# Optimization experiments

Measured on AMD Instinct MI355X. Metric: run time of the kernel, lower is better.

## Reference

```python
import jax, jax.numpy as jnp
import numpy as np

B, N, C = 256, 25, 256          # batch, joints, in_features
H = 256                          # hidden_features (MLP hidden = H // 2 = 128)


def _build_chain_paths(n):
    """Flatten shortest paths of a chain skeleton (parent[i]=i-1) into
    (heads, ends, pair_ids): edge k of path i->j contributes
    src[:, ends[e]] - src[:, heads[e]] accumulated into pair i*n+j."""
    heads, ends, pair = [], [], []
    for i in range(n):
        for j in range(n):
            step = 1 if j >= i else -1
            cur = i
            while cur != j:
                heads.append(cur)
                ends.append(cur + step)
                pair.append(i * n + j)
                cur += step
    return (np.asarray(heads, np.int32), np.asarray(ends, np.int32),
            np.asarray(pair, np.int32))


def setup_inputs() -> dict:
    key = jax.random.key(0)
    k_src, k_w1, k_w2 = jax.random.split(key, 3)
    heads, ends, pair_ids = _build_chain_paths(N)  # E = 5200 for N=25
    src = jax.random.normal(k_src, (B, N, C), dtype=jnp.float32)
    # torch Linear weights: [out, in], no bias for both edgefeat linears
    W1 = jax.random.normal(k_w1, (H // 2, C), dtype=jnp.float32) / np.sqrt(C)
    W2 = jax.random.normal(k_w2, (1, H // 2), dtype=jnp.float32) / np.sqrt(H // 2)
    alpha = jnp.full((1,), 0.25, dtype=jnp.float32)  # PReLU init
    return {"src": src, "heads": jnp.asarray(heads), "ends": jnp.asarray(ends),
            "pair_ids": jnp.asarray(pair_ids), "W1": W1, "alpha": alpha, "W2": W2}


def reference(src, heads, ends, pair_ids, W1, alpha, W2):
    b, n, c = src.shape
    # gather-subtract along every path edge: [B, E, C]
    diff = src[:, ends, :] - src[:, heads, :]
    # accumulate per (i, j) pair: segment_sum over leading axis -> [N*N, B, C]
    acc = jax.ops.segment_sum(jnp.transpose(diff, (1, 0, 2)), pair_ids,
                              num_segments=n * n)
    edge_feat = jnp.transpose(acc.reshape(n, n, b, c), (2, 0, 1, 3))  # [B,N,N,C]
    h = jnp.einsum('bijc,hc->bijh', edge_feat, W1)   # [B,N,N,H//2]
    h = jnp.where(h >= 0, h, alpha * h)              # PReLU (single shared alpha)
    return jnp.einsum('bijh,oh->bijo', h, W2)        # [B,N,N,1]
```

## Files before the change

kernel.cpp:

```cpp
#include <hip/hip_runtime.h>

#define NJ   25
#define CIN  256
#define HH   128
#define SS   264
#define US   136

typedef _Float16 h2  __attribute__((ext_vector_type(2)));
typedef _Float16 h8f __attribute__((ext_vector_type(8)));
typedef __attribute__((ext_vector_type(4))) float f32x4;

__device__ __forceinline__ unsigned short f2h_bits(float f) {
    union { _Float16 h; unsigned short u; } v; v.h = (_Float16)f; return v.u;
}
__device__ __forceinline__ unsigned pack2h(float a, float b) {
    return (unsigned)f2h_bits(a) | ((unsigned)f2h_bits(b) << 16);
}
__device__ __forceinline__ h2 as_h2(unsigned u) {
    union { unsigned u; h2 h; } v; v.u = u; return v.h;
}

__global__ __launch_bounds__(512) void fused_edge_mlp_v10(
    const float* __restrict__ src,
    const float* __restrict__ W1,
    const float* __restrict__ Aarr,
    const float* __restrict__ W2,
    float* __restrict__ out)
{
    __shared__ unsigned short s_lds[NJ * SS];
    __shared__ unsigned short u16[NJ * US];
    __shared__ unsigned w2s[HH / 2];
    __shared__ float s_s[NJ];

    const int b    = blockIdx.x;
    const int t    = threadIdx.x;
    const int w    = t >> 6;
    const int lane = t & 63;
    const int ln15 = lane & 15;
    const int quad = lane >> 4;
    const int hcol = w * 16 + ln15;

    const float* w1row = W1 + (size_t)hcol * CIN + quad * 8;
    float4 w1r[16];
    #pragma unroll
    for (int kt = 0; kt < 8; ++kt) {
        w1r[2 * kt]     = *(const float4*)(w1row + kt * 32);
        w1r[2 * kt + 1] = *(const float4*)(w1row + kt * 32 + 4);
    }

    const float4* s4 = (const float4*)(src + (size_t)b * NJ * CIN);
    float4 sv[4];
    #pragma unroll
    for (int it = 0; it < 4; ++it) {
        const int idx = t + it * 512;
        if (idx < NJ * CIN / 4) sv[it] = s4[idx];
    }
    if (t < HH / 2) w2s[t] = pack2h(W2[2 * t], W2[2 * t + 1]);

    #pragma unroll
    for (int it = 0; it < 4; ++it) {
        const int idx = t + it * 512;
        if (idx < NJ * CIN / 4) {
            const int n = idx >> 6, k4 = idx & 63;
            *(uint2*)&s_lds[n * SS + k4 * 4] =
                make_uint2(pack2h(sv[it].x, sv[it].y), pack2h(sv[it].z, sv[it].w));
        }
    }

    h8f bfr[8];
    #pragma unroll
    for (int kt = 0; kt < 8; ++kt) {
        const float4 lo = w1r[2 * kt], hi = w1r[2 * kt + 1];
        h8f f;
        f[0] = (_Float16)lo.x; f[1] = (_Float16)lo.y;
        f[2] = (_Float16)lo.z; f[3] = (_Float16)lo.w;
        f[4] = (_Float16)hi.x; f[5] = (_Float16)hi.y;
        f[6] = (_Float16)hi.z; f[7] = (_Float16)hi.w;
        bfr[kt] = f;
    }
    __syncthreads();

    {
        const int r1    = 16 + ln15;
        const bool r1ok = (r1 < NJ);
        const int cbase = quad * 8;

        f32x4 acc0 = {0.f, 0.f, 0.f, 0.f};
        f32x4 acc1 = {0.f, 0.f, 0.f, 0.f};
        #pragma unroll
        for (int kt = 0; kt < 8; ++kt) {
            const int co = kt * 32 + cbase;
            h8f a0 = *(const h8f*)&s_lds[ln15 * SS + co];
            h8f a1 = {};
            if (r1ok) a1 = *(const h8f*)&s_lds[r1 * SS + co];
            acc0 = __builtin_amdgcn_mfma_f32_16x16x32_f16(a0, bfr[kt], acc0, 0, 0, 0);
            acc1 = __builtin_amdgcn_mfma_f32_16x16x32_f16(a1, bfr[kt], acc1, 0, 0, 0);
        }

        #pragma unroll
        for (int r = 0; r < 4; ++r) {
            int m0 = quad * 4 + r;
            if (m0 < NJ) u16[m0 * US + hcol] = f2h_bits(acc0[r]);
            int m1 = 16 + quad * 4 + r;
            if (m1 < NJ) u16[m1 * US + hcol] = f2h_bits(acc1[r]);
        }
    }
    __syncthreads();

    const float alpha = Aarr[0];
    float* outb = out + (size_t)b * (NJ * NJ);
    const uint4* w2v = (const uint4*)w2s;

    float M = 0.f;
    int i = 0, j = 0;
    if (t < 300) {
        i = (int)((49.0f - sqrtf(2401.0f - 8.0f * (float)t)) * 0.5f);
        {
            int Si = (49 * i - i * i) >> 1;
            if (t < Si) { --i; }
            else { int Sn = (49 * (i + 1) - (i + 1) * (i + 1)) >> 1; if (t >= Sn) ++i; }
        }
        const int S = (49 * i - i * i) >> 1;
        j = t - S + i + 1;

        const uint4* ujp = (const uint4*)(u16 + j * US);
        const uint4* uip = (const uint4*)(u16 + i * US);
        #pragma unroll
        for (int h8 = 0; h8 < 16; ++h8) {
            uint4 a = ujp[h8], c = uip[h8], ww = w2v[h8];
            h2 mx;
            mx = __builtin_elementwise_max(as_h2(a.x), as_h2(c.x));
            M  = __builtin_amdgcn_fdot2(mx, as_h2(ww.x), M, false);
            mx = __builtin_elementwise_max(as_h2(a.y), as_h2(c.y));
            M  = __builtin_amdgcn_fdot2(mx, as_h2(ww.y), M, false);
            mx = __builtin_elementwise_max(as_h2(a.z), as_h2(c.z));
            M  = __builtin_amdgcn_fdot2(mx, as_h2(ww.z), M, false);
            mx = __builtin_elementwise_max(as_h2(a.w), as_h2(c.w));
            M  = __builtin_amdgcn_fdot2(mx, as_h2(ww.w), M, false);
        }
    } else if (t < 300 + NJ) {
        const int r = t - 300;
        const uint4* up = (const uint4*)(u16 + r * US);
        float s = 0.f;
        #pragma unroll
        for (int h8 = 0; h8 < 16; ++h8) {
            uint4 a = up[h8], ww = w2v[h8];
            s = __builtin_amdgcn_fdot2(as_h2(a.x), as_h2(ww.x), s, false);
            s = __builtin_amdgcn_fdot2(as_h2(a.y), as_h2(ww.y), s, false);
            s = __builtin_amdgcn_fdot2(as_h2(a.z), as_h2(ww.z), s, false);
            s = __builtin_amdgcn_fdot2(as_h2(a.w), as_h2(ww.w), s, false);
        }
        s_s[r] = s;
    }
    __syncthreads();

    if (t < 300) {
        const float sj = s_s[j], si = s_s[i];
        const float Mw = (1.f - alpha) * M;
        outb[i * NJ + j] = Mw + alpha * sj - si;
        outb[j * NJ + i] = Mw + alpha * si - sj;
    } else if (t >= 325 && t < 350) {
        const int r = t - 325;
        outb[r * (NJ + 1)] = 0.f;
    }
}

extern "C" void kernel_launch(void* const* d_in, const int* in_sizes, int n_in,
                              void* d_out, int out_size, void* d_ws, size_t ws_size,
                              hipStream_t stream) {
    const float* src   = (const float*)d_in[0];
    const float* W1    = (const float*)d_in[4];
    const float* alpha = (const float*)d_in[5];
    const float* W2    = (const float*)d_in[6];
    float* out = (float*)d_out;

    const int B = in_sizes[0] / (NJ * CIN);
    fused_edge_mlp_v10<<<B, 512, 0, stream>>>(src, W1, alpha, W2, out);
}
```

Before: 72.14 us.

## Split each batch across two 256-thread blocks and inline row sums into pair loop

Launches two 256-thread blocks per batch element instead of one 512-thread block. Each wave now computes two 16-column halves of the hidden projection. Each block handles half of the 300 upper-triangle pairs. The separate per-row dot-product phase and its extra barrier are removed; each pair thread recomputes the i and j row sums inline. The intent is more blocks in flight and one fewer sync. In exchange, both blocks redo the full src load and GEMM for the same batch element, and the pair threads do extra redundant dot products.

```diff
diff --git a/kernel.cpp b/kernel.cpp
--- a/kernel.cpp
+++ b/kernel.cpp
@@ -20,7 +20,48 @@
     union { unsigned u; h2 h; } v; v.u = u; return v.h;
 }
 
-__global__ __launch_bounds__(512) void fused_edge_mlp_v10(
+__device__ __forceinline__ void do_pair(int p, const unsigned short* u16p,
+                                        const uint4* w2v, float alpha,
+                                        float* __restrict__ outb) {
+    int i = (int)((49.0f - sqrtf(2401.0f - 8.0f * (float)p)) * 0.5f);
+    {
+        int Si = (49 * i - i * i) >> 1;
+        if (p < Si) { --i; }
+        else { int Sn = (49 * (i + 1) - (i + 1) * (i + 1)) >> 1; if (p >= Sn) ++i; }
+    }
+    const int S = (49 * i - i * i) >> 1;
+    const int j = p - S + i + 1;
+
+    const uint4* ujp = (const uint4*)(u16p + j * US);
+    const uint4* uip = (const uint4*)(u16p + i * US);
+    float M = 0.f, sj = 0.f, si = 0.f;
+    #pragma unroll
+    for (int h8 = 0; h8 < 16; ++h8) {
+        uint4 a = ujp[h8], c = uip[h8], ww = w2v[h8];
+        h2 mx;
+        mx = __builtin_elementwise_max(as_h2(a.x), as_h2(c.x));
+        M  = __builtin_amdgcn_fdot2(mx, as_h2(ww.x), M, false);
+        sj = __builtin_amdgcn_fdot2(as_h2(a.x), as_h2(ww.x), sj, false);
+        si = __builtin_amdgcn_fdot2(as_h2(c.x), as_h2(ww.x), si, false);
+        mx = __builtin_elementwise_max(as_h2(a.y), as_h2(c.y));
+        M  = __builtin_amdgcn_fdot2(mx, as_h2(ww.y), M, false);
+        sj = __builtin_amdgcn_fdot2(as_h2(a.y), as_h2(ww.y), sj, false);
+        si = __builtin_amdgcn_fdot2(as_h2(c.y), as_h2(ww.y), si, false);
+        mx = __builtin_elementwise_max(as_h2(a.z), as_h2(c.z));
+        M  = __builtin_amdgcn_fdot2(mx, as_h2(ww.z), M, false);
+        sj = __builtin_amdgcn_fdot2(as_h2(a.z), as_h2(ww.z), sj, false);
+        si = __builtin_amdgcn_fdot2(as_h2(c.z), as_h2(ww.z), si, false);
+        mx = __builtin_elementwise_max(as_h2(a.w), as_h2(c.w));
+        M  = __builtin_amdgcn_fdot2(mx, as_h2(ww.w), M, false);
+        sj = __builtin_amdgcn_fdot2(as_h2(a.w), as_h2(ww.w), sj, false);
+        si = __builtin_amdgcn_fdot2(as_h2(c.w), as_h2(ww.w), si, false);
+    }
+    const float Mw = (1.f - alpha) * M;
+    outb[i * NJ + j] = Mw + alpha * sj - si;
+    outb[j * NJ + i] = Mw + alpha * si - sj;
+}
+
+__global__ __launch_bounds__(256, 2) void fused_edge_mlp_v11(
     const float* __restrict__ src,
     const float* __restrict__ W1,
     const float* __restrict__ Aarr,
@@ -30,36 +71,39 @@
     __shared__ unsigned short s_lds[NJ * SS];
     __shared__ unsigned short u16[NJ * US];
     __shared__ unsigned w2s[HH / 2];
-    __shared__ float s_s[NJ];
 
-    const int b    = blockIdx.x;
+    const int b    = blockIdx.x >> 1;
+    const int half = blockIdx.x & 1;
     const int t    = threadIdx.x;
     const int w    = t >> 6;
     const int lane = t & 63;
     const int ln15 = lane & 15;
     const int quad = lane >> 4;
-    const int hcol = w * 16 + ln15;
+    const int hA   = w * 16 + ln15;
+    const int hB   = 64 + hA;
 
-    const float* w1row = W1 + (size_t)hcol * CIN + quad * 8;
-    float4 w1r[16];
+    const float* wrA = W1 + (size_t)hA * CIN + quad * 8;
+    const float* wrB = W1 + (size_t)hB * CIN + quad * 8;
+    float4 w1a[16], w1b[16];
     #pragma unroll
     for (int kt = 0; kt < 8; ++kt) {
-        w1r[2 * kt]     = *(const float4*)(w1row + kt * 32);
-        w1r[2 * kt + 1] = *(const float4*)(w1row + kt * 32 + 4);
+        w1a[2 * kt]     = *(const float4*)(wrA + kt * 32);
+        w1a[2 * kt + 1] = *(const float4*)(wrA + kt * 32 + 4);
+        w1b[2 * kt]     = *(const float4*)(wrB + kt * 32);
+        w1b[2 * kt + 1] = *(const float4*)(wrB + kt * 32 + 4);
     }
 
     const float4* s4 = (const float4*)(src + (size_t)b * NJ * CIN);
-    float4 sv[4];
+    float4 sv[7];
     #pragma unroll
-    for (int it = 0; it < 4; ++it) {
-        const int idx = t + it * 512;
+    for (int it = 0; it < 7; ++it) {
+        const int idx = t + it * 256;
         if (idx < NJ * CIN / 4) sv[it] = s4[idx];
     }
     if (t < HH / 2) w2s[t] = pack2h(W2[2 * t], W2[2 * t + 1]);
-
     #pragma unroll
-    for (int it = 0; it < 4; ++it) {
-        const int idx = t + it * 512;
+    for (int it = 0; it < 7; ++it) {
+        const int idx = t + it * 256;
         if (idx < NJ * CIN / 4) {
             const int n = idx >> 6, k4 = idx & 63;
             *(uint2*)&s_lds[n * SS + k4 * 4] =
@@ -67,16 +111,26 @@
         }
     }
 
-    h8f bfr[8];
+    h8f bfa[8], bfb[8];
     #pragma unroll
     for (int kt = 0; kt < 8; ++kt) {
-        const float4 lo = w1r[2 * kt], hi = w1r[2 * kt + 1];
+        const float4 lo = w1a[2 * kt], hi = w1a[2 * kt + 1];
         h8f f;
         f[0] = (_Float16)lo.x; f[1] = (_Float16)lo.y;
         f[2] = (_Float16)lo.z; f[3] = (_Float16)lo.w;
         f[4] = (_Float16)hi.x; f[5] = (_Float16)hi.y;
         f[6] = (_Float16)hi.z; f[7] = (_Float16)hi.w;
-        bfr[kt] = f;
+        bfa[kt] = f;
+    }
+    #pragma unroll
+    for (int kt = 0; kt < 8; ++kt) {
+        const float4 lo = w1b[2 * kt], hi = w1b[2 * kt + 1];
+        h8f f;
+        f[0] = (_Float16)lo.x; f[1] = (_Float16)lo.y;
+        f[2] = (_Float16)lo.z; f[3] = (_Float16)lo.w;
+        f[4] = (_Float16)hi.x; f[5] = (_Float16)hi.y;
+        f[6] = (_Float16)hi.z; f[7] = (_Float16)hi.w;
+        bfb[kt] = f;
     }
     __syncthreads();
 
@@ -85,24 +139,34 @@
         const bool r1ok = (r1 < NJ);
         const int cbase = quad * 8;
 
-        f32x4 acc0 = {0.f, 0.f, 0.f, 0.f};
-        f32x4 acc1 = {0.f, 0.f, 0.f, 0.f};
+        f32x4 aA0 = {0.f, 0.f, 0.f, 0.f};
+        f32x4 aA1 = {0.f, 0.f, 0.f, 0.f};
+        f32x4 aB0 = {0.f, 0.f, 0.f, 0.f};
+        f32x4 aB1 = {0.f, 0.f, 0.f, 0.f};
         #pragma unroll
         for (int kt = 0; kt < 8; ++kt) {
             const int co = kt * 32 + cbase;
             h8f a0 = *(const h8f*)&s_lds[ln15 * SS + co];
             h8f a1 = {};
             if (r1ok) a1 = *(const h8f*)&s_lds[r1 * SS + co];
-            acc0 = __builtin_amdgcn_mfma_f32_16x16x32_f16(a0, bfr[kt], acc0, 0, 0, 0);
-            acc1 = __builtin_amdgcn_mfma_f32_16x16x32_f16(a1, bfr[kt], acc1, 0, 0, 0);
+            aA0 = __builtin_amdgcn_mfma_f32_16x16x32_f16(a0, bfa[kt], aA0, 0, 0, 0);
+            aA1 = __builtin_amdgcn_mfma_f32_16x16x32_f16(a1, bfa[kt], aA1, 0, 0, 0);
+            aB0 = __builtin_amdgcn_mfma_f32_16x16x32_f16(a0, bfb[kt], aB0, 0, 0, 0);
+            aB1 = __builtin_amdgcn_mfma_f32_16x16x32_f16(a1, bfb[kt], aB1, 0, 0, 0);
         }
 
         #pragma unroll
         for (int r = 0; r < 4; ++r) {
             int m0 = quad * 4 + r;
-            if (m0 < NJ) u16[m0 * US + hcol] = f2h_bits(acc0[r]);
+            if (m0 < NJ) {
+                u16[m0 * US + hA] = f2h_bits(aA0[r]);
+                u16[m0 * US + hB] = f2h_bits(aB0[r]);
+            }
             int m1 = 16 + quad * 4 + r;
-            if (m1 < NJ) u16[m1 * US + hcol] = f2h_bits(acc1[r]);
+            if (m1 < NJ) {
+                u16[m1 * US + hA] = f2h_bits(aA1[r]);
+                u16[m1 * US + hB] = f2h_bits(aB1[r]);
+            }
         }
     }
     __syncthreads();
@@ -111,58 +175,8 @@
     float* outb = out + (size_t)b * (NJ * NJ);
     const uint4* w2v = (const uint4*)w2s;
 
-    float M = 0.f;
-    int i = 0, j = 0;
-    if (t < 300) {
-        i = (int)((49.0f - sqrtf(2401.0f - 8.0f * (float)t)) * 0.5f);
-        {
-            int Si = (49 * i - i * i) >> 1;
-            if (t < Si) { --i; }
-            else { int Sn = (49 * (i + 1) - (i + 1) * (i + 1)) >> 1; if (t >= Sn) ++i; }
-        }
-        const int S = (49 * i - i * i) >> 1;
-        j = t - S + i + 1;
-
-        const uint4* ujp = (const uint4*)(u16 + j * US);
-        const uint4* uip = (const uint4*)(u16 + i * US);
-        #pragma unroll
-        for (int h8 = 0; h8 < 16; ++h8) {
-            uint4 a = ujp[h8], c = uip[h8], ww = w2v[h8];
-            h2 mx;
-            mx = __builtin_elementwise_max(as_h2(a.x), as_h2(c.x));
-            M  = __builtin_amdgcn_fdot2(mx, as_h2(ww.x), M, false);
-            mx = __builtin_elementwise_max(as_h2(a.y), as_h2(c.y));
-            M  = __builtin_amdgcn_fdot2(mx, as_h2(ww.y), M, false);
-            mx = __builtin_elementwise_max(as_h2(a.z), as_h2(c.z));
-            M  = __builtin_amdgcn_fdot2(mx, as_h2(ww.z), M, false);
-            mx = __builtin_elementwise_max(as_h2(a.w), as_h2(c.w));
-            M  = __builtin_amdgcn_fdot2(mx, as_h2(ww.w), M, false);
-        }
-    } else if (t < 300 + NJ) {
-        const int r = t - 300;
-        const uint4* up = (const uint4*)(u16 + r * US);
-        float s = 0.f;
-        #pragma unroll
-        for (int h8 = 0; h8 < 16; ++h8) {
-            uint4 a = up[h8], ww = w2v[h8];
-            s = __builtin_amdgcn_fdot2(as_h2(a.x), as_h2(ww.x), s, false);
-            s = __builtin_amdgcn_fdot2(as_h2(a.y), as_h2(ww.y), s, false);
-            s = __builtin_amdgcn_fdot2(as_h2(a.z), as_h2(ww.z), s, false);
-            s = __builtin_amdgcn_fdot2(as_h2(a.w), as_h2(ww.w), s, false);
-        }
-        s_s[r] = s;
-    }
-    __syncthreads();
-
-    if (t < 300) {
-        const float sj = s_s[j], si = s_s[i];
-        const float Mw = (1.f - alpha) * M;
-        outb[i * NJ + j] = Mw + alpha * sj - si;
-        outb[j * NJ + i] = Mw + alpha * si - sj;
-    } else if (t >= 325 && t < 350) {
-        const int r = t - 325;
-        outb[r * (NJ + 1)] = 0.f;
-    }
+    if (t < 150) do_pair(150 * half + t, u16, w2v, alpha, outb);
+    if (half == 0 && t < NJ) outb[t * (NJ + 1)] = 0.f;
 }
 
 extern "C" void kernel_launch(void* const* d_in, const int* in_sizes, int n_in,
@@ -175,5 +189,5 @@
     float* out = (float*)d_out;
 
     const int B = in_sizes[0] / (NJ * CIN);
-    fused_edge_mlp_v10<<<B, 512, 0, stream>>>(src, W1, alpha, W2, out);
+    fused_edge_mlp_v11<<<2 * B, 256, 0, stream>>>(src, W1, alpha, W2, out);
 }
```

Result: slower. 77.79 us (+7.8%).
